# Kernel optimization log

Hardware: AMD Instinct MI355X
Metric: run time of the kernel (lower is better)

Reference implementation:

```python
import jax, jax.numpy as jnp
import numpy as np

N = 100000   # nodes
E = 1600000  # edges (avg degree 16)
F = 64       # num_features
H = 32       # hidden_size
C = 2        # num_classes
BN_EPS = 1e-5


def setup_inputs() -> dict:
    key = jax.random.key(0)
    ks = jax.random.split(key, 16)
    s_in = 1.0 / np.sqrt(F)
    s_h = 1.0 / np.sqrt(H)
    s_l = 1.0 / np.sqrt(3 * H)
    return {
        "x": jax.random.normal(ks[0], (N, F), jnp.float32),
        "edge_index": jax.random.randint(ks[1], (2, E), 0, N, dtype=jnp.int32),
        "edge_weights": jax.random.uniform(ks[2], (E,), jnp.float32),
        # GCNConv 1
        "W1": jax.random.uniform(ks[3], (F, H), jnp.float32, -s_in, s_in),
        "b1": jnp.zeros((H,), jnp.float32),
        "g1": jnp.ones((H,), jnp.float32),
        "be1": jnp.zeros((H,), jnp.float32),
        # GCNConv 2
        "W2": jax.random.uniform(ks[4], (H, H), jnp.float32, -s_h, s_h),
        "b2": jnp.zeros((H,), jnp.float32),
        "g2": jnp.ones((H,), jnp.float32),
        "be2": jnp.zeros((H,), jnp.float32),
        # GCNConv 3
        "W3": jax.random.uniform(ks[5], (H, H), jnp.float32, -s_h, s_h),
        "b3": jnp.zeros((H,), jnp.float32),
        "g3": jnp.ones((H,), jnp.float32),
        "be3": jnp.zeros((H,), jnp.float32),
        # Final linear: (3H -> C)
        "Wl": jax.random.uniform(ks[6], (3 * H, C), jnp.float32, -s_l, s_l),
        "bl": jax.random.uniform(ks[7], (C,), jnp.float32, -s_l, s_l),
    }


def _gcn_conv(x, W, b, row, col, w, n):
    # PyG GCNConv: h = x @ W; symmetric normalization with self-loops; scatter-add; + bias
    h = x @ W                                            # [N, H]
    deg = jax.ops.segment_sum(w, col, num_segments=n)    # [N]
    dis = jnp.where(deg > 0, jax.lax.rsqrt(deg), 0.0)    # deg^{-1/2}
    norm = dis[row] * w * dis[col]                       # [E+N]
    msg = h[row] * norm[:, None]                         # gather + normalize
    out = jax.ops.segment_sum(msg, col, num_segments=n)  # scatter-add to targets
    return out + b


def _bn(x, gamma, beta):
    # BatchNorm1d with batch statistics (biased variance), affine
    mu = x.mean(axis=0)
    var = x.var(axis=0)
    return (x - mu) * jax.lax.rsqrt(var + BN_EPS) * gamma + beta


def reference(x, edge_index, edge_weights,
              W1, b1, g1, be1,
              W2, b2, g2, be2,
              W3, b3, g3, be3,
              Wl, bl):
    n = x.shape[0]
    loops = jnp.arange(n, dtype=edge_index.dtype)
    row = jnp.concatenate([edge_index[0], loops])        # sources + self-loops
    col = jnp.concatenate([edge_index[1], loops])        # targets + self-loops
    w = jnp.concatenate([edge_weights, jnp.ones((n,), edge_weights.dtype)])

    out1 = _bn(jax.nn.relu(_gcn_conv(x, W1, b1, row, col, w, n)), g1, be1)
    out2 = _bn(jax.nn.relu(_gcn_conv(out1, W2, b2, row, col, w, n)), g2, be2)
    out3 = _bn(jax.nn.relu(_gcn_conv(out2, W3, b3, row, col, w, n)), g3, be3)

    rep = jnp.concatenate([out1, out2, out3], axis=1)    # [N, 3H]
    return rep @ Wl + bl                                 # [N, C]
```

## Files before the change

kernel.cpp:

```cpp
#include <hip/hip_runtime.h>

typedef unsigned int uint;
typedef unsigned char uchar;
typedef unsigned short ushort;
typedef unsigned long long ull;

#define F_IN 64
#define HD 32
#define NCLS 2
#define BN_EPS 1e-5f
#define SCHUNK 1024
#define NCOPY 8
#define FIX_SCALE 1073741824.0f
#define FIX_INV   9.313225746154785e-10f
#define MASK40 ((1ULL << 40) - 1)

__device__ __forceinline__ ull ld64(const int2* p) {
    return *reinterpret_cast<const ull*>(p);
}
__device__ __forceinline__ ushort f2bf(float f) {
    uint u = __float_as_uint(f);
    u = (u + 0x7FFFu + ((u >> 16) & 1u)) >> 16;
    return (ushort)u;
}
__device__ __forceinline__ float bf2f(ushort b) {
    return __uint_as_float((uint)b << 16);
}
__device__ __forceinline__ uchar f2e4(float x) {
    uint u = __float_as_uint(x);
    uint s = u & 0x80000000u;
    uint mag = u & 0x7fffffffu;
    if (mag < 0x3c800000u) return (uchar)(s >> 24);
    if (mag > 0x43e00000u) mag = 0x43e00000u;
    uint r = mag + 0x000FFFFFu + ((mag >> 20) & 1u);
    if (r > 0x43e00000u) r = 0x43e00000u;
    uint E = r >> 23;
    return (uchar)((s >> 24) | ((E - 120u) << 3) | ((r >> 20) & 7u));
}
__device__ __forceinline__ float e42f(uchar b) {
    uint s = ((uint)b & 0x80u) << 24;
    uint rest = (uint)b & 0x7fu;
    return __uint_as_float(s | ((rest << 20) + 0x3c000000u));
}

__global__ void hist64_kernel(const int* __restrict__ ei, const float* __restrict__ w,
                              ull* __restrict__ packed8, ushort* __restrict__ epos,
                              int E, int n) {
    int e = blockIdx.x * blockDim.x + threadIdx.x;
    if (e >= E) return;
    int k = blockIdx.x & (NCOPY - 1);
    int c = ei[E + e];
    ull fx = (ull)(w[e] * FIX_SCALE + 0.5f);
    ull old = atomicAdd(&packed8[(size_t)k * n + c], (1ULL << 40) | fx);
    epos[e] = (ushort)(old >> 40);
}

__global__ void scanA_kernel(const ull* __restrict__ packed8,
                             int* __restrict__ partial, float* __restrict__ dis, int n) {
    __shared__ int red[256];
    int base = blockIdx.x * SCHUNK;
    int tid = threadIdx.x;
    int s = 0;
    for (int i = tid; i < SCHUNK; i += 256) {
        int idx = base + i;
        if (idx < n) {
            int cnt = 0;
            ull fxs = 0;
#pragma unroll
            for (int k = 0; k < NCOPY; k++) {
                ull p = packed8[(size_t)k * n + idx];
                cnt += (int)(p >> 40);
                fxs += (p & MASK40);
            }
            s += cnt;
            float deg = (float)fxs * FIX_INV;
            dis[idx] = rsqrtf(deg + 1.0f);
        }
    }
    red[tid] = s;
    __syncthreads();
    for (int off = 128; off > 0; off >>= 1) {
        if (tid < off) red[tid] += red[tid + off];
        __syncthreads();
    }
    if (tid == 0) partial[blockIdx.x] = red[0];
}

__global__ void scanC_kernel(const ull* __restrict__ packed8, const int* __restrict__ partial,
                             int* __restrict__ offs, int* __restrict__ base8, int n, int scb) {
    __shared__ int lds[256];
    __shared__ int chunkBase, totalE;
    int tid = threadIdx.x;
    int v = (tid < scb) ? partial[tid] : 0;
    lds[tid] = v;
    __syncthreads();
    for (int off = 1; off < 256; off <<= 1) {
        int t = (tid >= off) ? lds[tid - off] : 0;
        __syncthreads();
        lds[tid] += t;
        __syncthreads();
    }
    if (tid == 0) {
        chunkBase = lds[blockIdx.x] - partial[blockIdx.x];
        totalE = lds[scb - 1];
    }
    __syncthreads();
    int i0 = blockIdx.x * SCHUNK + tid * 4;
    int cnt[4][NCOPY];
    int tot[4] = {0, 0, 0, 0};
#pragma unroll
    for (int t = 0; t < 4; t++) {
        int idx = i0 + t;
#pragma unroll
        for (int k = 0; k < NCOPY; k++) {
            int c = (idx < n) ? (int)(packed8[(size_t)k * n + idx] >> 40) : 0;
            cnt[t][k] = c;
            tot[t] += c;
        }
    }
    int tsum = tot[0] + tot[1] + tot[2] + tot[3];
    lds[tid] = tsum;
    __syncthreads();
    for (int off = 1; off < 256; off <<= 1) {
        int t = (tid >= off) ? lds[tid - off] : 0;
        __syncthreads();
        lds[tid] += t;
        __syncthreads();
    }
    int run = chunkBase + lds[tid] - tsum;
#pragma unroll
    for (int t = 0; t < 4; t++) {
        int idx = i0 + t;
        if (idx < n) {
            offs[idx] = run;
            int b = run;
#pragma unroll
            for (int k = 0; k < NCOPY; k++) {
                base8[(size_t)idx * NCOPY + k] = b;
                b += cnt[t][k];
            }
            run = b;
        }
    }
    if (blockIdx.x == 0 && tid == 0) offs[n] = totalE;
}

__global__ void fill_gemm1_kernel(const int* __restrict__ ei, const float* __restrict__ w,
                                  const int* __restrict__ base8, const ushort* __restrict__ epos,
                                  int2* __restrict__ centry, int E, int eb,
                                  const float* __restrict__ X, const float* __restrict__ W,
                                  const float* __restrict__ dis, ushort* __restrict__ Hb,
                                  float* __restrict__ statsCur, int n) {
    if ((int)blockIdx.x < eb) {
        int e = blockIdx.x * blockDim.x + threadIdx.x;
        if (e >= E) return;
        int k = blockIdx.x & (NCOPY - 1);
        int r = ei[e], c = ei[E + e];
        int pos = base8[(size_t)c * NCOPY + k] + (int)epos[e];
        centry[pos] = make_int2(r, __float_as_int(w[e]));
        return;
    }
    __shared__ float Wl[F_IN * HD];
    int gb = (int)blockIdx.x - eb;
    for (int i = threadIdx.x; i < F_IN * HD; i += blockDim.x) Wl[i] = W[i];
    if (gb == 0) {
        for (int i = threadIdx.x; i < NCOPY * 64; i += blockDim.x) statsCur[i] = 0.0f;
    }
    __syncthreads();
    int idx = gb * (int)blockDim.x + (int)threadIdx.x;
    if (idx >= n * HD) return;
    int node = idx >> 5, h = idx & 31;
    const float4* xr4 = reinterpret_cast<const float4*>(X + (size_t)node * F_IN);
    float acc = 0.0f;
#pragma unroll
    for (int q = 0; q < F_IN / 4; q++) {
        float4 v4 = xr4[q];
        float vs[4] = {v4.x, v4.y, v4.z, v4.w};
#pragma unroll
        for (int j = 0; j < 4; j++) {
            acc += vs[j] * Wl[(q * 4 + j) * HD + h];
        }
    }
    Hb[idx] = f2bf(acc * dis[node]);
}

template <bool FP8>
__global__ void gemm_bn_kernel(const float* __restrict__ X, const float* __restrict__ W,
                               const float* __restrict__ statsPrev, const float* __restrict__ g,
                               const float* __restrict__ be, const float* __restrict__ dis,
                               ushort* __restrict__ Hb, uchar* __restrict__ Hb8,
                               float* __restrict__ statsCur, int n) {
    __shared__ float Wl[HD * HD];
    __shared__ float scl[64];
    for (int i = threadIdx.x; i < HD * HD; i += blockDim.x) Wl[i] = W[i];
    if (threadIdx.x < 32) {
        int h = threadIdx.x;
        float sm = 0.f, sq = 0.f;
#pragma unroll
        for (int k = 0; k < NCOPY; k++) {
            sm += statsPrev[k * 64 + h];
            sq += statsPrev[k * 64 + 32 + h];
        }
        float invn = 1.0f / (float)n;
        float mean = sm * invn;
        float var = sq * invn - mean * mean;
        float sca = rsqrtf(var + BN_EPS) * g[h];
        scl[h] = sca;
        scl[32 + h] = be[h] - mean * sca;
    }
    if (blockIdx.x == 0) {
        for (int i = threadIdx.x; i < NCOPY * 64; i += blockDim.x) statsCur[i] = 0.0f;
    }
    __syncthreads();
    int idx = blockIdx.x * blockDim.x + threadIdx.x;
    if (idx >= n * HD) return;
    int node = idx >> 5, h = idx & 31;
    const float4* xr4 = reinterpret_cast<const float4*>(X + (size_t)node * HD);
    float acc = 0.0f;
#pragma unroll
    for (int q = 0; q < HD / 4; q++) {
        float4 v4 = xr4[q];
        float vs[4] = {v4.x, v4.y, v4.z, v4.w};
#pragma unroll
        for (int j = 0; j < 4; j++) {
            int k = q * 4 + j;
            acc += (vs[j] * scl[k] + scl[32 + k]) * Wl[k * HD + h];
        }
    }
    float v = acc * dis[node];
    if (FP8) Hb8[idx] = f2e4(v * 16.0f);
    else     Hb[idx]  = f2bf(v);
}

__global__ void aggV4n_kernel(const ushort* __restrict__ hb, const int* __restrict__ offs,
                              const int2* __restrict__ centry, const float* __restrict__ dis,
                              const float* __restrict__ bias, float* __restrict__ y,
                              float* __restrict__ stats, int n) {
    const int NPW = 16;
    int wave = threadIdx.x >> 6, lane = threadIdx.x & 63, sub = lane >> 5, h = lane & 31;
    float bv = bias[h];
    float lsum = 0.f, lsq = 0.f;
    int base = (blockIdx.x * 4 + wave) * NPW;
    for (int t = 0; t < NPW; t++) {
        int node = base + t;
        if (node >= n) break;
        int s = offs[node], e2 = offs[node + 1];
        int len = e2 - s;
        int half = (len + 1) >> 1;
        int j    = sub ? (s + half) : s;
        int jend = sub ? e2 : (s + half);
        float dd = dis[node];
        float a0 = 0.f, a1 = 0.f, a2 = 0.f, a3 = 0.f;
        if (sub == 0) a0 = bf2f(hb[(size_t)node * HD + h]);
        for (; j + 3 < jend; j += 4) {
            ull p0 = ld64(centry + j);
            ull p1 = ld64(centry + j + 1);
            ull p2 = ld64(centry + j + 2);
            ull p3 = ld64(centry + j + 3);
            a0 += bf2f(hb[(size_t)(uint)p0 * HD + h]) * __uint_as_float((uint)(p0 >> 32));
            a1 += bf2f(hb[(size_t)(uint)p1 * HD + h]) * __uint_as_float((uint)(p1 >> 32));
            a2 += bf2f(hb[(size_t)(uint)p2 * HD + h]) * __uint_as_float((uint)(p2 >> 32));
            a3 += bf2f(hb[(size_t)(uint)p3 * HD + h]) * __uint_as_float((uint)(p3 >> 32));
        }
        for (; j < jend; j++) {
            ull p0 = ld64(centry + j);
            a0 += bf2f(hb[(size_t)(uint)p0 * HD + h]) * __uint_as_float((uint)(p0 >> 32));
        }
        a0 += a1 + a2 + a3;
        a0 += __shfl_xor(a0, 32, 64);
        float yv = fmaxf(fmaf(a0, dd, bv), 0.f);
        if (sub == 0) {
            y[(size_t)node * HD + h] = yv;
            lsum += yv; lsq += yv * yv;
        }
    }
    __shared__ float ls[4][32], lq[4][32];
    if (sub == 0) { ls[wave][h] = lsum; lq[wave][h] = lsq; }
    __syncthreads();
    if (threadIdx.x < 32) {
        int k = blockIdx.x & (NCOPY - 1);
        float a = ls[0][threadIdx.x] + ls[1][threadIdx.x] + ls[2][threadIdx.x] + ls[3][threadIdx.x];
        float b = lq[0][threadIdx.x] + lq[1][threadIdx.x] + lq[2][threadIdx.x] + lq[3][threadIdx.x];
        atomicAdd(&stats[k * 64 + threadIdx.x], a);
        atomicAdd(&stats[k * 64 + 32 + threadIdx.x], b);
    }
}

__global__ void aggV4n8_kernel(const uchar* __restrict__ hb8, const int* __restrict__ offs,
                               const int2* __restrict__ centry, const float* __restrict__ dis,
                               const float* __restrict__ bias, float* __restrict__ y,
                               float* __restrict__ stats, int n) {
    const int NPW = 16;
    int wave = threadIdx.x >> 6, lane = threadIdx.x & 63, sub = lane >> 5, h = lane & 31;
    float bv = bias[h];
    float lsum = 0.f, lsq = 0.f;
    int base = (blockIdx.x * 4 + wave) * NPW;
    for (int t = 0; t < NPW; t++) {
        int node = base + t;
        if (node >= n) break;
        int s = offs[node], e2 = offs[node + 1];
        int len = e2 - s;
        int half = (len + 1) >> 1;
        int j    = sub ? (s + half) : s;
        int jend = sub ? e2 : (s + half);
        float dd = dis[node] * 0.0625f;
        float a0 = 0.f, a1 = 0.f, a2 = 0.f, a3 = 0.f;
        if (sub == 0) a0 = e42f(hb8[(size_t)node * HD + h]);
        for (; j + 3 < jend; j += 4) {
            ull p0 = ld64(centry + j);
            ull p1 = ld64(centry + j + 1);
            ull p2 = ld64(centry + j + 2);
            ull p3 = ld64(centry + j + 3);
            a0 += e42f(hb8[(size_t)(uint)p0 * HD + h]) * __uint_as_float((uint)(p0 >> 32));
            a1 += e42f(hb8[(size_t)(uint)p1 * HD + h]) * __uint_as_float((uint)(p1 >> 32));
            a2 += e42f(hb8[(size_t)(uint)p2 * HD + h]) * __uint_as_float((uint)(p2 >> 32));
            a3 += e42f(hb8[(size_t)(uint)p3 * HD + h]) * __uint_as_float((uint)(p3 >> 32));
        }
        for (; j < jend; j++) {
            ull p0 = ld64(centry + j);
            a0 += e42f(hb8[(size_t)(uint)p0 * HD + h]) * __uint_as_float((uint)(p0 >> 32));
        }
        a0 += a1 + a2 + a3;
        a0 += __shfl_xor(a0, 32, 64);
        float yv = fmaxf(fmaf(a0, dd, bv), 0.f);
        if (sub == 0) {
            y[(size_t)node * HD + h] = yv;
            lsum += yv; lsq += yv * yv;
        }
    }
    __shared__ float ls[4][32], lq[4][32];
    if (sub == 0) { ls[wave][h] = lsum; lq[wave][h] = lsq; }
    __syncthreads();
    if (threadIdx.x < 32) {
        int k = blockIdx.x & (NCOPY - 1);
        float a = ls[0][threadIdx.x] + ls[1][threadIdx.x] + ls[2][threadIdx.x] + ls[3][threadIdx.x];
        float b = lq[0][threadIdx.x] + lq[1][threadIdx.x] + lq[2][threadIdx.x] + lq[3][threadIdx.x];
        atomicAdd(&stats[k * 64 + threadIdx.x], a);
        atomicAdd(&stats[k * 64 + 32 + threadIdx.x], b);
    }
}

__global__ void final_kernel(const float* __restrict__ y1, const float* __restrict__ y2,
                             const float* __restrict__ y3,
                             const float* __restrict__ s1, const float* __restrict__ s2,
                             const float* __restrict__ s3,
                             const float* __restrict__ g1, const float* __restrict__ be1,
                             const float* __restrict__ g2, const float* __restrict__ be2,
                             const float* __restrict__ g3, const float* __restrict__ be3,
                             const float* __restrict__ Wl, const float* __restrict__ bl,
                             float* __restrict__ out, int n) {
    __shared__ float Ws[96 * NCLS];
    __shared__ float scs[3][64];
    __shared__ float bs[NCLS];
    for (int i = threadIdx.x; i < 96 * NCLS; i += blockDim.x) Ws[i] = Wl[i];
    if (threadIdx.x < 96) {
        int L = threadIdx.x >> 5, h = threadIdx.x & 31;
        const float* st = (L == 0) ? s1 : (L == 1) ? s2 : s3;
        const float* gg = (L == 0) ? g1 : (L == 1) ? g2 : g3;
        const float* bb = (L == 0) ? be1 : (L == 1) ? be2 : be3;
        float sm = 0.f, sq = 0.f;
#pragma unroll
        for (int k = 0; k < NCOPY; k++) {
            sm += st[k * 64 + h];
            sq += st[k * 64 + 32 + h];
        }
        float invn = 1.0f / (float)n;
        float mean = sm * invn;
        float var = sq * invn - mean * mean;
        float sca = rsqrtf(var + BN_EPS) * gg[h];
        scs[L][h] = sca;
        scs[L][32 + h] = bb[h] - mean * sca;
    }
    if (threadIdx.x < NCLS) bs[threadIdx.x] = bl[threadIdx.x];
    __syncthreads();
    int i = blockIdx.x * blockDim.x + threadIdx.x;
    if (i >= n) return;
    float a0 = bs[0], a1 = bs[1];
    const float* ys[3] = {y1 + (size_t)i * HD, y2 + (size_t)i * HD, y3 + (size_t)i * HD};
#pragma unroll
    for (int L = 0; L < 3; L++) {
        const float4* r4 = reinterpret_cast<const float4*>(ys[L]);
#pragma unroll
        for (int q = 0; q < HD / 4; q++) {
            float4 v4 = r4[q];
            float vs[4] = {v4.x, v4.y, v4.z, v4.w};
#pragma unroll
            for (int j = 0; j < 4; j++) {
                int h = q * 4 + j;
                float v = vs[j] * scs[L][h] + scs[L][32 + h];
                a0 += v * Ws[(L * 32 + h) * 2];
                a1 += v * Ws[(L * 32 + h) * 2 + 1];
            }
        }
    }
    out[(size_t)i * 2] = a0;
    out[(size_t)i * 2 + 1] = a1;
}

extern "C" void kernel_launch(void* const* d_in, const int* in_sizes, int n_in,
                              void* d_out, int out_size, void* d_ws, size_t ws_size,
                              hipStream_t stream) {
    const float* x  = (const float*)d_in[0];
    const int*   ei = (const int*)d_in[1];
    const float* ew = (const float*)d_in[2];
    const float* W1 = (const float*)d_in[3];  const float* b1  = (const float*)d_in[4];
    const float* g1 = (const float*)d_in[5];  const float* be1 = (const float*)d_in[6];
    const float* W2 = (const float*)d_in[7];  const float* b2  = (const float*)d_in[8];
    const float* g2 = (const float*)d_in[9];  const float* be2 = (const float*)d_in[10];
    const float* W3 = (const float*)d_in[11]; const float* b3  = (const float*)d_in[12];
    const float* g3 = (const float*)d_in[13]; const float* be3 = (const float*)d_in[14];
    const float* Wl = (const float*)d_in[15]; const float* bl  = (const float*)d_in[16];

    int n = in_sizes[0] / F_IN;
    int E = in_sizes[1] / 2;

    char* ws = (char*)d_ws;
    auto alloc = [&](size_t bytes) -> char* {
        char* p = ws;
        ws += (bytes + 255) / 256 * 256;
        return p;
    };
    ull*    packed8 = (ull*)alloc((size_t)NCOPY * n * 8);
    float*  dis     = (float*)alloc((size_t)n * 4);
    int*    offs    = (int*)alloc((size_t)(n + 1) * 4);
    int*    base8   = (int*)alloc((size_t)n * NCOPY * 4);
    int*    partial = (int*)alloc(256 * 4);
    ushort* epos    = (ushort*)alloc((size_t)E * 2);
    int2*   centry  = (int2*)alloc((size_t)E * 8);
    ushort* hb      = (ushort*)alloc((size_t)n * HD * 2);
    uchar*  hb8     = (uchar*)alloc((size_t)n * HD);
    float*  y1      = (float*)alloc((size_t)n * HD * 4);
    float*  y2      = (float*)alloc((size_t)n * HD * 4);
    float*  y3      = (float*)alloc((size_t)n * HD * 4);
    float*  stats1  = (float*)alloc(NCOPY * 64 * 4);
    float*  stats2  = (float*)alloc(NCOPY * 64 * 4);
    float*  stats3  = (float*)alloc(NCOPY * 64 * 4);

    hipMemsetAsync(packed8, 0, (size_t)NCOPY * n * 8, stream);

    int eb  = (E + 255) / 256;
    int nb  = (n + 255) / 256;
    int nhb = (n * HD + 255) / 256;
    int scb = (n + SCHUNK - 1) / SCHUNK;
    int agb = (n + 63) / 64;

    hist64_kernel<<<eb, 256, 0, stream>>>(ei, ew, packed8, epos, E, n);
    scanA_kernel<<<scb, 256, 0, stream>>>(packed8, partial, dis, n);
    scanC_kernel<<<scb, 256, 0, stream>>>(packed8, partial, offs, base8, n, scb);

    fill_gemm1_kernel<<<eb + nhb, 256, 0, stream>>>(ei, ew, base8, epos, centry, E, eb,
                                                    x, W1, dis, hb, stats1, n);

    aggV4n_kernel<<<agb, 256, 0, stream>>>(hb, offs, centry, dis, b1, y1, stats1, n);
    gemm_bn_kernel<true><<<nhb, 256, 0, stream>>>(y1, W2, stats1, g1, be1, dis, hb, hb8, stats2, n);
    aggV4n8_kernel<<<agb, 256, 0, stream>>>(hb8, offs, centry, dis, b2, y2, stats2, n);
    gemm_bn_kernel<false><<<nhb, 256, 0, stream>>>(y2, W3, stats2, g3, be3, dis, hb, hb8, stats3, n);
    aggV4n_kernel<<<agb, 256, 0, stream>>>(hb, offs, centry, dis, b3, y3, stats3, n);

    final_kernel<<<nb, 256, 0, stream>>>(y1, y2, y3, stats1, stats2, stats3,
                                         g1, be1, g2, be2, g3, be3, Wl, bl, (float*)d_out, n);
}
```

Before: 376.6 us.

## Partition CSR edges by source half and split layer-3 aggregation into two passes

The histogram and fill kernels now choose the copy slot from whether the source node lies in the lower or upper half of the node range, so each destination's edge list is grouped by source half. The third aggregation runs as two kernels: the first gathers only from lower-half sources into a scratch accumulator, and the second gathers from upper-half sources, adds the partial sum and applies bias, ReLU and the BN statistics. The goal is to shrink the gather working set of bf16 hidden rows in each pass so it fits better in cache. In exchange it adds a kernel launch, an extra fp32 N×H write and read, and fewer copies for spreading atomic contention in the histogram.

```diff
diff --git a/kernel.cpp b/kernel.cpp
--- a/kernel.cpp
+++ b/kernel.cpp
@@ -45,11 +45,12 @@
 
 __global__ void hist64_kernel(const int* __restrict__ ei, const float* __restrict__ w,
                               ull* __restrict__ packed8, ushort* __restrict__ epos,
-                              int E, int n) {
+                              int E, int n, int halfn) {
     int e = blockIdx.x * blockDim.x + threadIdx.x;
     if (e >= E) return;
-    int k = blockIdx.x & (NCOPY - 1);
+    int r = ei[e];
     int c = ei[E + e];
+    int k = ((r >= halfn) ? 4 : 0) | ((int)blockIdx.x & 3);
     ull fx = (ull)(w[e] * FIX_SCALE + 0.5f);
     ull old = atomicAdd(&packed8[(size_t)k * n + c], (1ULL << 40) | fx);
     epos[e] = (ushort)(old >> 40);
@@ -147,15 +148,15 @@
 
 __global__ void fill_gemm1_kernel(const int* __restrict__ ei, const float* __restrict__ w,
                                   const int* __restrict__ base8, const ushort* __restrict__ epos,
-                                  int2* __restrict__ centry, int E, int eb,
+                                  int2* __restrict__ centry, int E, int eb, int halfn,
                                   const float* __restrict__ X, const float* __restrict__ W,
                                   const float* __restrict__ dis, ushort* __restrict__ Hb,
                                   float* __restrict__ statsCur, int n) {
     if ((int)blockIdx.x < eb) {
         int e = blockIdx.x * blockDim.x + threadIdx.x;
         if (e >= E) return;
-        int k = blockIdx.x & (NCOPY - 1);
         int r = ei[e], c = ei[E + e];
+        int k = ((r >= halfn) ? 4 : 0) | ((int)blockIdx.x & 3);
         int pos = base8[(size_t)c * NCOPY + k] + (int)epos[e];
         centry[pos] = make_int2(r, __float_as_int(w[e]));
         return;
@@ -286,6 +287,97 @@
     }
 }
 
+__global__ void aggP0_kernel(const ushort* __restrict__ hb, const int* __restrict__ offs,
+                             const int* __restrict__ base8, const int2* __restrict__ centry,
+                             float* __restrict__ yacc, int n) {
+    const int NPW = 16;
+    int wave = threadIdx.x >> 6, lane = threadIdx.x & 63, sub = lane >> 5, h = lane & 31;
+    int base = (blockIdx.x * 4 + wave) * NPW;
+    for (int t = 0; t < NPW; t++) {
+        int node = base + t;
+        if (node >= n) break;
+        int s = offs[node], e2 = base8[(size_t)node * NCOPY + 4];
+        int len = e2 - s;
+        int half = (len + 1) >> 1;
+        int j    = sub ? (s + half) : s;
+        int jend = sub ? e2 : (s + half);
+        float a0 = 0.f, a1 = 0.f, a2 = 0.f, a3 = 0.f;
+        for (; j + 3 < jend; j += 4) {
+            ull p0 = ld64(centry + j);
+            ull p1 = ld64(centry + j + 1);
+            ull p2 = ld64(centry + j + 2);
+            ull p3 = ld64(centry + j + 3);
+            a0 += bf2f(hb[(size_t)(uint)p0 * HD + h]) * __uint_as_float((uint)(p0 >> 32));
+            a1 += bf2f(hb[(size_t)(uint)p1 * HD + h]) * __uint_as_float((uint)(p1 >> 32));
+            a2 += bf2f(hb[(size_t)(uint)p2 * HD + h]) * __uint_as_float((uint)(p2 >> 32));
+            a3 += bf2f(hb[(size_t)(uint)p3 * HD + h]) * __uint_as_float((uint)(p3 >> 32));
+        }
+        for (; j < jend; j++) {
+            ull p0 = ld64(centry + j);
+            a0 += bf2f(hb[(size_t)(uint)p0 * HD + h]) * __uint_as_float((uint)(p0 >> 32));
+        }
+        a0 += a1 + a2 + a3;
+        a0 += __shfl_xor(a0, 32, 64);
+        if (sub == 0) yacc[(size_t)node * HD + h] = a0;
+    }
+}
+
+__global__ void aggP1_kernel(const ushort* __restrict__ hb, const int* __restrict__ offs,
+                             const int* __restrict__ base8, const int2* __restrict__ centry,
+                             const float* __restrict__ dis, const float* __restrict__ bias,
+                             const float* __restrict__ yacc, float* __restrict__ y,
+                             float* __restrict__ stats, int n) {
+    const int NPW = 16;
+    int wave = threadIdx.x >> 6, lane = threadIdx.x & 63, sub = lane >> 5, h = lane & 31;
+    float bv = bias[h];
+    float lsum = 0.f, lsq = 0.f;
+    int base = (blockIdx.x * 4 + wave) * NPW;
+    for (int t = 0; t < NPW; t++) {
+        int node = base + t;
+        if (node >= n) break;
+        int s = base8[(size_t)node * NCOPY + 4], e2 = offs[node + 1];
+        int len = e2 - s;
+        int half = (len + 1) >> 1;
+        int j    = sub ? (s + half) : s;
+        int jend = sub ? e2 : (s + half);
+        float dd = dis[node];
+        float a0 = 0.f, a1 = 0.f, a2 = 0.f, a3 = 0.f;
+        if (sub == 0) a0 = bf2f(hb[(size_t)node * HD + h]);
+        for (; j + 3 < jend; j += 4) {
+            ull p0 = ld64(centry + j);
+            ull p1 = ld64(centry + j + 1);
+            ull p2 = ld64(centry + j + 2);
+            ull p3 = ld64(centry + j + 3);
+            a0 += bf2f(hb[(size_t)(uint)p0 * HD + h]) * __uint_as_float((uint)(p0 >> 32));
+            a1 += bf2f(hb[(size_t)(uint)p1 * HD + h]) * __uint_as_float((uint)(p1 >> 32));
+            a2 += bf2f(hb[(size_t)(uint)p2 * HD + h]) * __uint_as_float((uint)(p2 >> 32));
+            a3 += bf2f(hb[(size_t)(uint)p3 * HD + h]) * __uint_as_float((uint)(p3 >> 32));
+        }
+        for (; j < jend; j++) {
+            ull p0 = ld64(centry + j);
+            a0 += bf2f(hb[(size_t)(uint)p0 * HD + h]) * __uint_as_float((uint)(p0 >> 32));
+        }
+        a0 += a1 + a2 + a3;
+        a0 += __shfl_xor(a0, 32, 64);
+        if (sub == 0) {
+            float tot = a0 + yacc[(size_t)node * HD + h];
+            float yv = fmaxf(fmaf(tot, dd, bv), 0.f);
+            y[(size_t)node * HD + h] = yv;
+            lsum += yv; lsq += yv * yv;
+        }
+    }
+    __shared__ float ls[4][32], lq[4][32];
+    if (sub == 0) { ls[wave][h] = lsum; lq[wave][h] = lsq; }
+    __syncthreads();
+    if (threadIdx.x < 32) {
+        int k = blockIdx.x & (NCOPY - 1);
+        float a = ls[0][threadIdx.x] + ls[1][threadIdx.x] + ls[2][threadIdx.x] + ls[3][threadIdx.x];
+        float b = lq[0][threadIdx.x] + lq[1][threadIdx.x] + lq[2][threadIdx.x] + lq[3][threadIdx.x];
+        atomicAdd(&stats[k * 64 + threadIdx.x], a);
+        atomicAdd(&stats[k * 64 + 32 + threadIdx.x], b);
+    }
+}
+
 __global__ void aggV4n8_kernel(const uchar* __restrict__ hb8, const int* __restrict__ offs,
                                const int2* __restrict__ centry, const float* __restrict__ dis,
                                const float* __restrict__ bias, float* __restrict__ y,
@@ -413,6 +505,7 @@
 
     int n = in_sizes[0] / F_IN;
     int E = in_sizes[1] / 2;
+    int halfn = n >> 1;
 
     char* ws = (char*)d_ws;
     auto alloc = [&](size_t bytes) -> char* {
@@ -432,6 +525,7 @@
     float*  y1      = (float*)alloc((size_t)n * HD * 4);
     float*  y2      = (float*)alloc((size_t)n * HD * 4);
     float*  y3      = (float*)alloc((size_t)n * HD * 4);
+    float*  yacc    = (float*)alloc((size_t)n * HD * 4);
     float*  stats1  = (float*)alloc(NCOPY * 64 * 4);
     float*  stats2  = (float*)alloc(NCOPY * 64 * 4);
     float*  stats3  = (float*)alloc(NCOPY * 64 * 4);
@@ -444,18 +538,19 @@
     int scb = (n + SCHUNK - 1) / SCHUNK;
     int agb = (n + 63) / 64;
 
-    hist64_kernel<<<eb, 256, 0, stream>>>(ei, ew, packed8, epos, E, n);
+    hist64_kernel<<<eb, 256, 0, stream>>>(ei, ew, packed8, epos, E, n, halfn);
     scanA_kernel<<<scb, 256, 0, stream>>>(packed8, partial, dis, n);
     scanC_kernel<<<scb, 256, 0, stream>>>(packed8, partial, offs, base8, n, scb);
 
-    fill_gemm1_kernel<<<eb + nhb, 256, 0, stream>>>(ei, ew, base8, epos, centry, E, eb,
+    fill_gemm1_kernel<<<eb + nhb, 256, 0, stream>>>(ei, ew, base8, epos, centry, E, eb, halfn,
                                                     x, W1, dis, hb, stats1, n);
 
     aggV4n_kernel<<<agb, 256, 0, stream>>>(hb, offs, centry, dis, b1, y1, stats1, n);
     gemm_bn_kernel<true><<<nhb, 256, 0, stream>>>(y1, W2, stats1, g1, be1, dis, hb, hb8, stats2, n);
     aggV4n8_kernel<<<agb, 256, 0, stream>>>(hb8, offs, centry, dis, b2, y2, stats2, n);
     gemm_bn_kernel<false><<<nhb, 256, 0, stream>>>(y2, W3, stats2, g3, be3, dis, hb, hb8, stats3, n);
-    aggV4n_kernel<<<agb, 256, 0, stream>>>(hb, offs, centry, dis, b3, y3, stats3, n);
+    aggP0_kernel<<<agb, 256, 0, stream>>>(hb, offs, base8, centry, yacc, n);
+    aggP1_kernel<<<agb, 256, 0, stream>>>(hb, offs, base8, centry, dis, b3, yacc, y3, stats3, n);
 
     final_kernel<<<nb, 256, 0, stream>>>(y1, y2, y3, stats1, stats2, stats3,
                                          g1, be1, g2, be2, g3, be3, Wl, bl, (float*)d_out, n);
```

Measured after the change: 410.0 us. +8.9%, slower.
